# Optimization experiments

Measured on AMD Instinct MI355X. Metric: run time of the kernel, lower is better.

The kernel has to match this reference:

```python
import jax, jax.numpy as jnp
import numpy as np

N = 20000       # nodes
E = 160000      # edges (avg degree 8)
NFEAT = 512
NHID = 512
NCLASS = 64
NLAYERS = 4


def setup_inputs() -> dict:
    key = jax.random.key(0)
    ks = jax.random.split(key, 9)
    s = 0.05
    x = jax.random.normal(ks[0], (N, NFEAT), dtype=jnp.float32)
    edge_index = jax.random.randint(ks[1], (2, E), 0, N, dtype=jnp.int64)
    W_enc = jax.random.normal(ks[2], (NFEAT, NHID), dtype=jnp.float32) * s
    b_enc = jnp.zeros((NHID,), dtype=jnp.float32)
    W_convs = jax.random.normal(ks[3], (NLAYERS, NHID, NHID), dtype=jnp.float32) * s
    b_convs = jnp.zeros((NLAYERS, NHID), dtype=jnp.float32)
    W_dec = jax.random.normal(ks[4], (NHID, NCLASS), dtype=jnp.float32) * s
    b_dec = jnp.zeros((NCLASS,), dtype=jnp.float32)
    return {"x": x, "edge_index": edge_index, "W_enc": W_enc, "b_enc": b_enc,
            "W_convs": W_convs, "b_convs": b_convs, "W_dec": W_dec, "b_dec": b_dec}


def reference(x, edge_index, W_enc, b_enc, W_convs, b_convs, W_dec, b_dec):
    n = x.shape[0]
    loops = jnp.arange(n, dtype=edge_index.dtype)
    # GCNConv adds self-loops, then sym-normalizes: D^-1/2 (A+I) D^-1/2
    src = jnp.concatenate([edge_index[0], loops])  # [E+N]
    dst = jnp.concatenate([edge_index[1], loops])  # [E+N]
    deg = jax.ops.segment_sum(jnp.ones_like(dst, dtype=x.dtype), dst, num_segments=N)
    dinv = jnp.where(deg > 0, jax.lax.rsqrt(deg), jnp.zeros_like(deg))
    norm = (dinv[src] * dinv[dst])[:, None]  # [E+N, 1]

    # encoder: relu(Linear)
    h = jax.nn.relu(x @ W_enc + b_enc)

    def gcn_step(h, wb):
        W, b = wb
        hW = h @ W                                   # [N, H]
        msg = hW[src] * norm                         # gather + scale
        agg = jax.ops.segment_sum(msg, dst, num_segments=N)  # scatter-add
        return jax.nn.relu(agg + b), None            # bias after aggregation (PyG)

    h, _ = jax.lax.scan(gcn_step, h, (W_convs, b_convs))

    # decoder (dropout p=0 in eval -> identity)
    return h @ W_dec + b_dec
```

## Files before the change

### kernel.cpp

```cpp
#include <hip/hip_runtime.h>

#define N_NODES 20000
#define E_EDGES 160000
#define NFEAT   512
#define NHID    512
#define NCLASS  64
#define NLAYERS 4

#define SCAN_CHUNK 1024
#define NBLK ((N_NODES + SCAN_CHUNK - 1) / SCAN_CHUNK)
#define CNT_BLOCKS ((E_EDGES + 255) / 256)
#define CVT_BLOCKS ((N_NODES * NFEAT) / 2048)

using bf16x8 = __attribute__((ext_vector_type(8))) short;
using f32x4  = __attribute__((ext_vector_type(4))) float;
using u16x8  = __attribute__((ext_vector_type(8))) unsigned short;

__device__ __forceinline__ unsigned short f2bf(float f) {
    union { float f; unsigned int u; } v; v.f = f;
    unsigned int u = v.u + 0x7FFFu + ((v.u >> 16) & 1u);
    return (unsigned short)(u >> 16);
}
__device__ __forceinline__ float bf2f(unsigned short h) {
    union { unsigned int u; float f; } v; v.u = ((unsigned int)h) << 16;
    return v.f;
}
__device__ __forceinline__ void gl2lds16(const void* gptr, void* lptr) {
    __builtin_amdgcn_global_load_lds(
        (const __attribute__((address_space(1))) unsigned int*)gptr,
        (__attribute__((address_space(3))) unsigned int*)lptr,
        16, 0, 0);
}

__global__ __launch_bounds__(256) void prep_all(const int* __restrict__ dst,
                                                int* __restrict__ counts,
                                                int* __restrict__ bsums,
                                                const float* __restrict__ W_enc,
                                                const float* __restrict__ W_convs,
                                                const float* __restrict__ W_dec,
                                                unsigned short* __restrict__ WencT,
                                                unsigned short* __restrict__ WcvT,
                                                unsigned short* __restrict__ WdecT,
                                                const float* __restrict__ x,
                                                unsigned short* __restrict__ Xbf) {
    __shared__ int bins[NBLK];
    __shared__ float tile[32][33];
    const int b = blockIdx.x, t = threadIdx.x;

    if (b < CNT_BLOCKS) {
        if (t < NBLK) bins[t] = 0;
        __syncthreads();
        const int e = b * 256 + t;
        if (e < E_EDGES) {
            const int d = dst[e];
            atomicAdd(&counts[d], 1);
            atomicAdd(&bins[d >> 10], 1);
        }
        __syncthreads();
        if (t < NBLK && bins[t]) atomicAdd(&bsums[t], bins[t]);
        return;
    }

    if (b >= CNT_BLOCKS + 6 * 256) {
        const int cid = b - CNT_BLOCKS - 6 * 256;
        const size_t base = (size_t)cid * 2048 + (size_t)t * 8;
        const float4 f0 = *(const float4*)(x + base);
        const float4 f1 = *(const float4*)(x + base + 4);
        u16x8 pk;
        pk[0] = f2bf(f0.x); pk[1] = f2bf(f0.y);
        pk[2] = f2bf(f0.z); pk[3] = f2bf(f0.w);
        pk[4] = f2bf(f1.x); pk[5] = f2bf(f1.y);
        pk[6] = f2bf(f1.z); pk[7] = f2bf(f1.w);
        *(u16x8*)(Xbf + base) = pk;
        return;
    }

    const int bid = b - CNT_BLOCKS;
    const int id  = bid >> 8;
    const int rem = bid & 255;
    const int n0  = (rem & 15) * 32;
    const int k0  = (rem >> 4) * 32;
    const float* W; unsigned short* WT; int N;
    const int K = 512;
    if (id == 0)            { W = W_enc; WT = WencT; N = NHID; }
    else if (id <= NLAYERS) { W = W_convs + (size_t)(id - 1) * NHID * NHID;
                              WT = WcvT  + (size_t)(id - 1) * NHID * NHID; N = NHID; }
    else                    { W = W_dec; WT = WdecT; N = NCLASS; }
    if (n0 >= N) return;
    const int tx = t & 31, ty = t >> 5;
#pragma unroll
    for (int i = 0; i < 32; i += 8)
        tile[ty + i][tx] = W[(size_t)(k0 + ty + i) * N + n0 + tx];
    __syncthreads();
#pragma unroll
    for (int i = 0; i < 32; i += 8)
        WT[(size_t)(n0 + ty + i) * K + k0 + tx] = f2bf(tile[tx][ty + i]);
}

__global__ __launch_bounds__(256) void write_rowptr(const int* __restrict__ counts,
                                                    const int* __restrict__ bsums,
                                                    int* __restrict__ row_ptr,
                                                    int* __restrict__ cursor,
                                                    float* __restrict__ dinv) {
    __shared__ int part[256];
    __shared__ int boff_s;
    const int b = blockIdx.x, t = threadIdx.x;

    if (t < 64) {
        int v = (t < NBLK && t < b) ? bsums[t] : 0;
        for (int off = 32; off > 0; off >>= 1) v += __shfl_xor(v, off, 64);
        if (t == 0) boff_s = v;
    }

    const int base = b * SCAN_CHUNK + t * 4;
    int c[4], s = 0;
    for (int i = 0; i < 4; ++i) {
        int idx = base + i;
        c[i] = (idx < N_NODES) ? counts[idx] : 0;
        s += c[i];
    }
    part[t] = s;
    __syncthreads();
    for (int off = 1; off < 256; off <<= 1) {
        int v = (t >= off) ? part[t - off] : 0;
        __syncthreads();
        part[t] += v;
        __syncthreads();
    }
    int run = boff_s + ((t == 0) ? 0 : part[t - 1]);
    for (int i = 0; i < 4; ++i) {
        int idx = base + i;
        if (idx < N_NODES) {
            row_ptr[idx] = run;
            cursor[idx]  = run;
            dinv[idx]    = rsqrtf((float)c[i] + 1.0f);
            run += c[i];
        }
    }
    if (b == 0 && t == 0) row_ptr[N_NODES] = E_EDGES;
}

__global__ __launch_bounds__(256) void csr_fill(const int* __restrict__ src,
                                                const int* __restrict__ dst,
                                                const float* __restrict__ dinv,
                                                int* __restrict__ cursor,
                                                int2* __restrict__ ew) {
    int e = blockIdx.x * 256 + threadIdx.x;
    if (e < E_EDGES) {
        int s = src[e], d = dst[e];
        int pos = atomicAdd(&cursor[d], 1);
        ew[pos] = make_int2(s, __float_as_int(dinv[s] * dinv[d]));
    }
    if (e < 8) ew[E_EDGES + e] = make_int2(0, 0);
}

template <int BM, int BN, int WR, int WC, bool RELU, bool HASBIAS, bool OUTBF16>
__global__ __launch_bounds__(256) void gemm_mfma(const unsigned short* __restrict__ A,
                                                 const unsigned short* __restrict__ BT,
                                                 const float* __restrict__ bias,
                                                 void* __restrict__ Cout,
                                                 int M, int N, int K) {
    constexpr int BK  = 32;
    constexpr int R   = BM / (16 * WR);
    constexpr int C   = BN / (16 * WC);
    constexpr int RA  = (BM * BK) / (256 * 8);
    constexpr int RB  = (BN * BK) / (256 * 8);
    constexpr int LPT = RA + RB;
    __shared__ unsigned short lA[2][BM * BK];
    __shared__ unsigned short lB[2][BN * BK];

    const int t    = threadIdx.x;
    const int lane = t & 63;
    const int wv   = t >> 6;
    const int wr   = wv / WC;
    const int wc   = wv % WC;
    const int lm   = lane & 15;
    const int quad = lane >> 4;

    const int MBLK = (M + BM - 1) / BM;
    const int NBN  = N / BN;
    int mblk, nblk;
    {
        const int i    = blockIdx.x;
        const int full = (MBLK / 8) * 8 * NBN;
        if (i < full) {
            const int g = i / (8 * NBN);
            const int l = i % (8 * NBN);
            mblk = g * 8 + (l & 7);
            nblk = l >> 3;
        } else {
            const int t2  = i - full;
            const int rem = MBLK - (MBLK / 8) * 8;
            mblk = (MBLK / 8) * 8 + t2 % rem;
            nblk = t2 / rem;
        }
    }
    const int m0 = mblk * BM;
    const int n0 = nblk * BN;

    f32x4 acc[R][C] = {};

    auto stage = [&](int s, int kt) {
#pragma unroll
        for (int i = 0; i < RA; ++i) {
            int idx = i * 256 + t;
            int row = idx >> 2;
            int kof = (idx & 3) << 3;
            int gr = m0 + row; if (gr >= M) gr = M - 1;
            gl2lds16(A + (size_t)gr * K + kt + kof, &lA[s][idx * 8]);
        }
#pragma unroll
        for (int i = 0; i < RB; ++i) {
            int idx = i * 256 + t;
            int row = idx >> 2;
            int kof = (idx & 3) << 3;
            gl2lds16(BT + (size_t)(n0 + row) * K + kt + kof, &lB[s][idx * 8]);
        }
    };

    stage(0, 0);
    int cur = 0;
    for (int kt = 0; kt < K; kt += BK) {
        if (kt + BK < K) {
            stage(cur ^ 1, kt + BK);
            asm volatile("s_waitcnt vmcnt(%0)" :: "i"(LPT) : "memory");
        } else {
            asm volatile("s_waitcnt vmcnt(0)" ::: "memory");
        }
        __builtin_amdgcn_sched_barrier(0);
        __builtin_amdgcn_s_barrier();

        bf16x8 af[R], bfr[C];
#pragma unroll
        for (int r = 0; r < R; ++r)
            af[r] = *(const bf16x8*)&lA[cur][(wr * R * 16 + r * 16 + lm) * BK + quad * 8];
#pragma unroll
        for (int c = 0; c < C; ++c)
            bfr[c] = *(const bf16x8*)&lB[cur][(wc * C * 16 + c * 16 + lm) * BK + quad * 8];
        asm volatile("s_waitcnt lgkmcnt(0)" ::: "memory");
        __builtin_amdgcn_sched_barrier(0);
#pragma unroll
        for (int r = 0; r < R; ++r)
#pragma unroll
            for (int c = 0; c < C; ++c)
                acc[r][c] = __builtin_amdgcn_mfma_f32_16x16x32_bf16(af[r], bfr[c],
                                                                    acc[r][c], 0, 0, 0);
        __builtin_amdgcn_sched_barrier(0);
        __builtin_amdgcn_s_barrier();
        cur ^= 1;
    }

#pragma unroll
    for (int r = 0; r < R; ++r) {
#pragma unroll
        for (int c = 0; c < C; ++c) {
            const int colg = n0 + wc * C * 16 + c * 16 + lm;
            const float bb = HASBIAS ? bias[colg] : 0.0f;
            const int rowb = m0 + wr * R * 16 + r * 16 + quad * 4;
#pragma unroll
            for (int i = 0; i < 4; ++i) {
                const int rr = rowb + i;
                if (rr < M) {
                    float v = acc[r][c][i] + bb;
                    if (RELU) v = fmaxf(v, 0.0f);
                    if (OUTBF16)
                        ((unsigned short*)Cout)[(size_t)rr * N + colg] = f2bf(v);
                    else
                        ((float*)Cout)[(size_t)rr * N + colg] = v;
                }
            }
        }
    }
}

__global__ __launch_bounds__(256) void gcn_aggregate(const unsigned short* __restrict__ hW,
                                                     const int* __restrict__ row_ptr,
                                                     const int2* __restrict__ ew,
                                                     const float* __restrict__ dinv,
                                                     const float* __restrict__ bias,
                                                     unsigned short* __restrict__ out) {
    const int wv   = threadIdx.x >> 6;
    const int lane = threadIdx.x & 63;
    int d = blockIdx.x * 2 + (wv >> 1);
    d = __builtin_amdgcn_readfirstlane(d);
    if (d >= N_NODES) return;
    const int fh = wv & 1;
    const int beg = __builtin_amdgcn_readfirstlane(row_ptr[d]);
    const int end = __builtin_amdgcn_readfirstlane(row_ptr[d + 1]);
    const size_t foff = (size_t)fh * 256 + (size_t)lane * 4;

    const float di = dinv[d];
    const float sl = di * di;
    const ushort4 sv = *(const ushort4*)(hW + (size_t)d * NHID + foff);
    float acc[4];
    acc[0] = bf2f(sv.x) * sl;
    acc[1] = bf2f(sv.y) * sl;
    acc[2] = bf2f(sv.z) * sl;
    acc[3] = bf2f(sv.w) * sl;

    for (int j = beg; j < end; j += 8) {
        int    sK[8];
        float  wK[8];
        ushort4 v[8];
#pragma unroll
        for (int k = 0; k < 8; ++k) {
            const int jj = j + k;
            const int2 e = ew[jj];
            const bool valid = jj < end;
            sK[k] = valid ? e.x : 0;
            wK[k] = valid ? __int_as_float(e.y) : 0.0f;
        }
#pragma unroll
        for (int k = 0; k < 8; ++k)
            v[k] = *(const ushort4*)(hW + (size_t)sK[k] * NHID + foff);
#pragma unroll
        for (int k = 0; k < 8; ++k) {
            acc[0] += bf2f(v[k].x) * wK[k];
            acc[1] += bf2f(v[k].y) * wK[k];
            acc[2] += bf2f(v[k].z) * wK[k];
            acc[3] += bf2f(v[k].w) * wK[k];
        }
    }

    const float4 bv = *(const float4*)(bias + foff);
    ushort4 r;
    r.x = f2bf(fmaxf(acc[0] + bv.x, 0.0f));
    r.y = f2bf(fmaxf(acc[1] + bv.y, 0.0f));
    r.z = f2bf(fmaxf(acc[2] + bv.z, 0.0f));
    r.w = f2bf(fmaxf(acc[3] + bv.w, 0.0f));
    *(ushort4*)(out + (size_t)d * NHID + foff) = r;
}

extern "C" void kernel_launch(void* const* d_in, const int* in_sizes, int n_in,
                              void* d_out, int out_size, void* d_ws, size_t ws_size,
                              hipStream_t stream) {
    const float* x       = (const float*)d_in[0];
    const int*   ei      = (const int*)d_in[1];
    const float* W_enc   = (const float*)d_in[2];
    const float* b_enc   = (const float*)d_in[3];
    const float* W_convs = (const float*)d_in[4];
    const float* b_convs = (const float*)d_in[5];
    const float* W_dec   = (const float*)d_in[6];
    const float* b_dec   = (const float*)d_in[7];
    float* out = (float*)d_out;

    const int* src = ei;
    const int* dst = ei + E_EDGES;

    char* ws = (char*)d_ws;
    auto alloc = [&](size_t bytes) {
        char* p = ws;
        ws += (bytes + 255) / 256 * 256;
        return p;
    };
    float* dinv     = (float*)alloc(N_NODES * 4);
    int*   counts   = (int*)  alloc((N_NODES + NBLK) * 4);
    int*   bsums    = counts + N_NODES;
    int*   row_ptr  = (int*)  alloc((N_NODES + 1) * 4);
    int*   cursor   = (int*)  alloc(N_NODES * 4);
    int2*  ew       = (int2*) alloc((E_EDGES + 8) * 8);
    unsigned short* WencT = (unsigned short*)alloc((size_t)NFEAT * NHID * 2);
    unsigned short* WcvT  = (unsigned short*)alloc((size_t)NLAYERS * NHID * NHID * 2);
    unsigned short* WdecT = (unsigned short*)alloc((size_t)NHID * NCLASS * 2);
    unsigned short* B1    = (unsigned short*)alloc((size_t)N_NODES * NHID * 2);
    unsigned short* B2    = (unsigned short*)alloc((size_t)N_NODES * NHID * 2);
    unsigned short* Xbf   = B2;

    hipMemsetAsync(counts, 0, (N_NODES + NBLK) * sizeof(int), stream);
    prep_all<<<CNT_BLOCKS + 6 * 256 + CVT_BLOCKS, 256, 0, stream>>>(
        dst, counts, bsums, W_enc, W_convs, W_dec, WencT, WcvT, WdecT, x, Xbf);
    write_rowptr<<<NBLK, 256, 0, stream>>>(counts, bsums, row_ptr, cursor, dinv);
    csr_fill<<<(E_EDGES + 255) / 256, 256, 0, stream>>>(src, dst, dinv, cursor, ew);

    const int MBLK64 = (N_NODES + 63) / 64;

    gemm_mfma<64, 128, 2, 2, true, true, true>
        <<<MBLK64 * (NHID / 128), 256, 0, stream>>>(
        Xbf, WencT, b_enc, B1, N_NODES, NHID, NFEAT);

    for (int L = 0; L < NLAYERS; ++L) {
        gemm_mfma<64, 128, 2, 2, false, false, true>
            <<<MBLK64 * (NHID / 128), 256, 0, stream>>>(
            B1, WcvT + (size_t)L * NHID * NHID, nullptr, B2, N_NODES, NHID, NHID);
        gcn_aggregate<<<(N_NODES + 1) / 2, 256, 0, stream>>>(
            B2, row_ptr, ew, dinv, b_convs + (size_t)L * NHID, B1);
    }

    gemm_mfma<64, 64, 2, 2, false, true, false>
        <<<MBLK64 * (NCLASS / 64), 256, 0, stream>>>(
        B1, WdecT, b_dec, out, N_NODES, NCLASS, NHID);
}
```

Baseline: 343.8 us.

## Split layer GEMM into column halves and overlap second half with aggregation

Each GCN layer's GEMM is split into two column halves. The first half runs alone, then a combined kernel computes the second-half GEMM blocks alongside aggregation of the first 256 feature columns, and a final kernel aggregates the remaining half. A third ping-pong buffer avoids read/write hazards between a layer's input and its output. The goal is to overlap the compute-bound GEMM with the memory-bound gather, at the cost of an extra launch per layer and one more N×512 bf16 buffer.

```diff
diff --git a/kernel.cpp b/kernel.cpp
--- a/kernel.cpp
+++ b/kernel.cpp
@@ -155,19 +155,21 @@
 }
 
 template <int BM, int BN, int WR, int WC, bool RELU, bool HASBIAS, bool OUTBF16>
-__global__ __launch_bounds__(256) void gemm_mfma(const unsigned short* __restrict__ A,
-                                                 const unsigned short* __restrict__ BT,
-                                                 const float* __restrict__ bias,
-                                                 void* __restrict__ Cout,
-                                                 int M, int N, int K) {
-    constexpr int BK  = 32;
-    constexpr int R   = BM / (16 * WR);
-    constexpr int C   = BN / (16 * WC);
-    constexpr int RA  = (BM * BK) / (256 * 8);
-    constexpr int RB  = (BN * BK) / (256 * 8);
-    constexpr int LPT = RA + RB;
-    __shared__ unsigned short lA[2][BM * BK];
-    __shared__ unsigned short lB[2][BN * BK];
+__device__ __forceinline__ void gemm_body(unsigned short* lA, unsigned short* lB,
+                                          int bid,
+                                          const unsigned short* __restrict__ A,
+                                          const unsigned short* __restrict__ BT,
+                                          const float* __restrict__ bias,
+                                          void* __restrict__ Cout,
+                                          int M, int N, int K, int OS) {
+    constexpr int BK   = 32;
+    constexpr int R    = BM / (16 * WR);
+    constexpr int C    = BN / (16 * WC);
+    constexpr int RA   = (BM * BK) / (256 * 8);
+    constexpr int RB   = (BN * BK) / (256 * 8);
+    constexpr int LPT  = RA + RB;
+    constexpr int SZA  = BM * BK;
+    constexpr int SZB  = BN * BK;
 
     const int t    = threadIdx.x;
     const int lane = t & 63;
@@ -181,15 +183,14 @@
     const int NBN  = N / BN;
     int mblk, nblk;
     {
-        const int i    = blockIdx.x;
         const int full = (MBLK / 8) * 8 * NBN;
-        if (i < full) {
-            const int g = i / (8 * NBN);
-            const int l = i % (8 * NBN);
+        if (bid < full) {
+            const int g = bid / (8 * NBN);
+            const int l = bid % (8 * NBN);
             mblk = g * 8 + (l & 7);
             nblk = l >> 3;
         } else {
-            const int t2  = i - full;
+            const int t2  = bid - full;
             const int rem = MBLK - (MBLK / 8) * 8;
             mblk = (MBLK / 8) * 8 + t2 % rem;
             nblk = t2 / rem;
@@ -207,14 +208,14 @@
             int row = idx >> 2;
             int kof = (idx & 3) << 3;
             int gr = m0 + row; if (gr >= M) gr = M - 1;
-            gl2lds16(A + (size_t)gr * K + kt + kof, &lA[s][idx * 8]);
+            gl2lds16(A + (size_t)gr * K + kt + kof, &lA[s * SZA + idx * 8]);
         }
 #pragma unroll
         for (int i = 0; i < RB; ++i) {
             int idx = i * 256 + t;
             int row = idx >> 2;
             int kof = (idx & 3) << 3;
-            gl2lds16(BT + (size_t)(n0 + row) * K + kt + kof, &lB[s][idx * 8]);
+            gl2lds16(BT + (size_t)(n0 + row) * K + kt + kof, &lB[s * SZB + idx * 8]);
         }
     };
 
@@ -233,10 +234,10 @@
         bf16x8 af[R], bfr[C];
 #pragma unroll
         for (int r = 0; r < R; ++r)
-            af[r] = *(const bf16x8*)&lA[cur][(wr * R * 16 + r * 16 + lm) * BK + quad * 8];
+            af[r] = *(const bf16x8*)&lA[cur * SZA + (wr * R * 16 + r * 16 + lm) * BK + quad * 8];
 #pragma unroll
         for (int c = 0; c < C; ++c)
-            bfr[c] = *(const bf16x8*)&lB[cur][(wc * C * 16 + c * 16 + lm) * BK + quad * 8];
+            bfr[c] = *(const bf16x8*)&lB[cur * SZB + (wc * C * 16 + c * 16 + lm) * BK + quad * 8];
         asm volatile("s_waitcnt lgkmcnt(0)" ::: "memory");
         __builtin_amdgcn_sched_barrier(0);
 #pragma unroll
@@ -264,30 +265,43 @@
                     float v = acc[r][c][i] + bb;
                     if (RELU) v = fmaxf(v, 0.0f);
                     if (OUTBF16)
-                        ((unsigned short*)Cout)[(size_t)rr * N + colg] = f2bf(v);
+                        ((unsigned short*)Cout)[(size_t)rr * OS + colg] = f2bf(v);
                     else
-                        ((float*)Cout)[(size_t)rr * N + colg] = v;
+                        ((float*)Cout)[(size_t)rr * OS + colg] = v;
                 }
             }
         }
     }
 }
 
-__global__ __launch_bounds__(256) void gcn_aggregate(const unsigned short* __restrict__ hW,
-                                                     const int* __restrict__ row_ptr,
-                                                     const int2* __restrict__ ew,
-                                                     const float* __restrict__ dinv,
-                                                     const float* __restrict__ bias,
-                                                     unsigned short* __restrict__ out) {
+template <int BM, int BN, int WR, int WC, bool RELU, bool HASBIAS, bool OUTBF16>
+__global__ __launch_bounds__(256) void gemm_k(const unsigned short* __restrict__ A,
+                                              const unsigned short* __restrict__ BT,
+                                              const float* __restrict__ bias,
+                                              void* __restrict__ Cout,
+                                              int M, int N, int K, int OS) {
+    __shared__ unsigned short lA[2 * BM * 32];
+    __shared__ unsigned short lB[2 * BN * 32];
+    gemm_body<BM, BN, WR, WC, RELU, HASBIAS, OUTBF16>(
+        lA, lB, blockIdx.x, A, BT, bias, Cout, M, N, K, OS);
+}
+
+__device__ __forceinline__ void agg_body(int blk,
+                                         const unsigned short* __restrict__ hW,
+                                         const int* __restrict__ row_ptr,
+                                         const int2* __restrict__ ew,
+                                         const float* __restrict__ dinv,
+                                         const float* __restrict__ bias,
+                                         unsigned short* __restrict__ out,
+                                         int foffBase) {
     const int wv   = threadIdx.x >> 6;
     const int lane = threadIdx.x & 63;
-    int d = blockIdx.x * 2 + (wv >> 1);
+    int d = blk * 4 + wv;
     d = __builtin_amdgcn_readfirstlane(d);
     if (d >= N_NODES) return;
-    const int fh = wv & 1;
     const int beg = __builtin_amdgcn_readfirstlane(row_ptr[d]);
     const int end = __builtin_amdgcn_readfirstlane(row_ptr[d + 1]);
-    const size_t foff = (size_t)fh * 256 + (size_t)lane * 4;
+    const size_t foff = (size_t)foffBase + (size_t)lane * 4;
 
     const float di = dinv[d];
     const float sl = di * di;
@@ -329,6 +343,35 @@
     r.z = f2bf(fmaxf(acc[2] + bv.z, 0.0f));
     r.w = f2bf(fmaxf(acc[3] + bv.w, 0.0f));
     *(ushort4*)(out + (size_t)d * NHID + foff) = r;
+}
+
+__global__ __launch_bounds__(256) void agg_k(const unsigned short* __restrict__ hW,
+                                             const int* __restrict__ row_ptr,
+                                             const int2* __restrict__ ew,
+                                             const float* __restrict__ dinv,
+                                             const float* __restrict__ bias,
+                                             unsigned short* __restrict__ out,
+                                             int foffBase) {
+    agg_body(blockIdx.x, hW, row_ptr, ew, dinv, bias, out, foffBase);
+}
+
+__global__ __launch_bounds__(256) void gemm_agg(
+        const unsigned short* __restrict__ A,
+        const unsigned short* __restrict__ BTh,
+        unsigned short* __restrict__ Ch, int M, int N, int K, int OS,
+        int gemmBlocks,
+        const unsigned short* __restrict__ hW, const int* __restrict__ row_ptr,
+        const int2* __restrict__ ew, const float* __restrict__ dinv,
+        const float* __restrict__ abias, unsigned short* __restrict__ aout,
+        int foffBase) {
+    __shared__ unsigned short lA[2 * 64 * 32];
+    __shared__ unsigned short lB[2 * 128 * 32];
+    if (blockIdx.x < gemmBlocks)
+        gemm_body<64, 128, 2, 2, false, false, true>(
+            lA, lB, blockIdx.x, A, BTh, nullptr, Ch, M, N, K, OS);
+    else
+        agg_body(blockIdx.x - gemmBlocks, hW, row_ptr, ew, dinv, abias, aout,
+                 foffBase);
 }
 
 extern "C" void kernel_launch(void* const* d_in, const int* in_sizes, int n_in,
@@ -364,7 +407,8 @@
     unsigned short* WdecT = (unsigned short*)alloc((size_t)NHID * NCLASS * 2);
     unsigned short* B1    = (unsigned short*)alloc((size_t)N_NODES * NHID * 2);
     unsigned short* B2    = (unsigned short*)alloc((size_t)N_NODES * NHID * 2);
-    unsigned short* Xbf   = B2;
+    unsigned short* B3    = (unsigned short*)alloc((size_t)N_NODES * NHID * 2);
+    unsigned short* Xbf   = B3;
 
     hipMemsetAsync(counts, 0, (N_NODES + NBLK) * sizeof(int), stream);
     prep_all<<<CNT_BLOCKS + 6 * 256 + CVT_BLOCKS, 256, 0, stream>>>(
@@ -373,20 +417,30 @@
     csr_fill<<<(E_EDGES + 255) / 256, 256, 0, stream>>>(src, dst, dinv, cursor, ew);
 
     const int MBLK64 = (N_NODES + 63) / 64;
-
-    gemm_mfma<64, 128, 2, 2, true, true, true>
+    const int GH     = MBLK64 * 2;
+    const int AH     = (N_NODES + 3) / 4;
+
+    gemm_k<64, 128, 2, 2, true, true, true>
         <<<MBLK64 * (NHID / 128), 256, 0, stream>>>(
-        Xbf, WencT, b_enc, B1, N_NODES, NHID, NFEAT);
+        Xbf, WencT, b_enc, B1, N_NODES, NHID, NFEAT, NHID);
 
     for (int L = 0; L < NLAYERS; ++L) {
-        gemm_mfma<64, 128, 2, 2, false, false, true>
-            <<<MBLK64 * (NHID / 128), 256, 0, stream>>>(
-            B1, WcvT + (size_t)L * NHID * NHID, nullptr, B2, N_NODES, NHID, NHID);
-        gcn_aggregate<<<(N_NODES + 1) / 2, 256, 0, stream>>>(
-            B2, row_ptr, ew, dinv, b_convs + (size_t)L * NHID, B1);
-    }
-
-    gemm_mfma<64, 64, 2, 2, false, true, false>
+        const unsigned short* in  = (L & 1) ? B3 : B1;
+        unsigned short*       op  = (L & 1) ? B1 : B3;
+        const unsigned short* Wl  = WcvT + (size_t)L * NHID * NHID;
+        const float*          bl  = b_convs + (size_t)L * NHID;
+
+        gemm_k<64, 128, 2, 2, false, false, true>
+            <<<GH, 256, 0, stream>>>(in, Wl, nullptr, B2,
+                                     N_NODES, NHID / 2, NHID, NHID);
+        gemm_agg<<<GH + AH, 256, 0, stream>>>(
+            in, Wl + (size_t)(NHID / 2) * NHID, B2 + NHID / 2,
+            N_NODES, NHID / 2, NHID, NHID, GH,
+            B2, row_ptr, ew, dinv, bl, op, 0);
+        agg_k<<<AH, 256, 0, stream>>>(B2, row_ptr, ew, dinv, bl, op, NHID / 2);
+    }
+
+    gemm_k<64, 64, 2, 2, false, true, false>
         <<<MBLK64 * (NCLASS / 64), 256, 0, stream>>>(
-        B1, WdecT, b_dec, out, N_NODES, NCLASS, NHID);
-}
+        B1, WdecT, b_dec, out, N_NODES, NCLASS, NHID, NCLASS);
+}
```

Result: slower. 361.4 us (+5.1%).
